# Kernel tuning notes

Hardware: AMD Instinct MI355X
Metric: run time of the kernel (lower is better)

## Reference

```python
import jax, jax.numpy as jnp
import numpy as np

B, T, V, E, U = 64, 256, 32000, 512, 1024


def setup_inputs() -> dict:
    key = jax.random.key(0)
    k1, k2, k3 = jax.random.split(key, 3)
    tokens = jax.random.randint(k1, (B, T), 0, V)
    hidden = jnp.zeros((B, U), dtype=jnp.float32)
    emb = jax.random.normal(k2, (V, E), dtype=jnp.float32) * 0.05
    kx, kh = jax.random.split(k3)
    # Keras GRU v2: kernel [E, 3U], recurrent_kernel [U, 3U], reset_after=True -> two bias vectors
    Wx = jax.random.normal(kx, (E, 3 * U), dtype=jnp.float32) * 0.02
    bx = jnp.zeros((3 * U,), dtype=jnp.float32)
    Wh = jax.random.normal(kh, (U, 3 * U), dtype=jnp.float32) * 0.02
    bh = jnp.zeros((3 * U,), dtype=jnp.float32)
    return {"tokens": tokens, "hidden": hidden, "emb": emb,
            "Wx": Wx, "bx": bx, "Wh": Wh, "bh": bh}


def _gru_scan(x_proj, h0, Wh, bh, units):
    # x_proj: [T, B, 3U] precomputed input projections (incl. input bias)
    def step(h, xt):
        rec = h @ Wh + bh                      # [B, 3U]
        xz, xr, xh = jnp.split(xt, 3, axis=-1)
        hz, hr, hh = jnp.split(rec, 3, axis=-1)
        z = jax.nn.sigmoid(xz + hz)
        r = jax.nn.sigmoid(xr + hr)
        cand = jnp.tanh(xh + r * hh)           # reset_after=True: r applied after matmul
        h_new = z * h + (1.0 - z) * cand
        return h_new, h_new
    h_last, seq = jax.lax.scan(step, h0, x_proj)
    return seq, h_last


def reference(tokens, hidden, emb, Wx, bx, Wh, bh):
    x = emb[tokens]                            # [B, T, E] embedding lookup
    x_proj = jnp.einsum('bte,eu->btu', x, Wx) + bx  # [B, T, 3U]
    seq, h_last = _gru_scan(jnp.swapaxes(x_proj, 0, 1), hidden, Wh, bh, U)
    output = jnp.swapaxes(seq, 0, 1)           # [B, T, U]
    return output, h_last
```

## Files before the change

### kernel.cpp

```cpp
#include <hip/hip_runtime.h>
#include <cstdint>

typedef _Float16 f16x8 __attribute__((ext_vector_type(8)));
typedef float    f32x4 __attribute__((ext_vector_type(4)));
typedef unsigned int u32;

#define BB 64
#define TT 256
#define EE 512
#define UU 1024
#define NN 3072

#define MFMA16(a, b, c) __builtin_amdgcn_mfma_f32_16x16x32_f16((a), (b), (c), 0, 0, 0)

__global__ __launch_bounds__(256) void prep_whf(const float* __restrict__ Wh,
                                                _Float16* __restrict__ WhF) {
    int tid  = blockIdx.x * 256 + threadIdx.x;
    int col8 = tid % 384;
    int k    = tid / 384;
    int kb = k >> 5, quad = (k >> 3) & 3, jj = k & 7;
    const float* src = Wh + (long)k * NN + col8 * 8;
#pragma unroll
    for (int i = 0; i < 8; i++) {
        int n   = col8 * 8 + i;
        int g   = n >> 10;
        int nl  = n & 1023;
        int j   = nl >> 4, l16 = nl & 15;
        int lane = quad * 16 + l16;
        WhF[((((j * 3 + g) * 32 + kb) * 64 + lane) << 3) + jj] = (_Float16)src[i];
    }
}

__global__ __launch_bounds__(256) void prep_h0(const float* __restrict__ h0,
                                               _Float16* __restrict__ hbuf) {
    int i = blockIdx.x * 256 + threadIdx.x;
    hbuf[i] = (_Float16)h0[i];
}

__global__ __launch_bounds__(256) void proj_kernel(
    const int* __restrict__ tokens, const float* __restrict__ emb,
    const float* __restrict__ Wx, const float* __restrict__ bx,
    _Float16* __restrict__ xproj) {
    int tid  = threadIdx.x;
    int wave = tid >> 6, lane = tid & 63, quad = lane >> 4, l16 = lane & 15;
    int bm = blockIdx.x * 64;
    int bn = blockIdx.y * 128;
    int wm = (wave & 1) * 32, wn = (wave >> 1) * 64;

    int row0 = bm + wm + l16;
    const float* a0p = emb + (long)tokens[row0] * EE;
    const float* a1p = emb + (long)tokens[row0 + 16] * EE;

    f32x4 acc[2][4];
#pragma unroll
    for (int mt = 0; mt < 2; mt++)
#pragma unroll
        for (int nt = 0; nt < 4; nt++) { f32x4 z = {0.f, 0.f, 0.f, 0.f}; acc[mt][nt] = z; }

#pragma unroll 2
    for (int k0 = 0; k0 < EE; k0 += 32) {
        int ka = k0 + quad * 8;
        f16x8 afr[2];
        {
            const float4* p = (const float4*)(a0p + ka);
            float4 x0 = p[0], x1 = p[1];
            afr[0][0] = (_Float16)x0.x; afr[0][1] = (_Float16)x0.y;
            afr[0][2] = (_Float16)x0.z; afr[0][3] = (_Float16)x0.w;
            afr[0][4] = (_Float16)x1.x; afr[0][5] = (_Float16)x1.y;
            afr[0][6] = (_Float16)x1.z; afr[0][7] = (_Float16)x1.w;
        }
        {
            const float4* p = (const float4*)(a1p + ka);
            float4 x0 = p[0], x1 = p[1];
            afr[1][0] = (_Float16)x0.x; afr[1][1] = (_Float16)x0.y;
            afr[1][2] = (_Float16)x0.z; afr[1][3] = (_Float16)x0.w;
            afr[1][4] = (_Float16)x1.x; afr[1][5] = (_Float16)x1.y;
            afr[1][6] = (_Float16)x1.z; afr[1][7] = (_Float16)x1.w;
        }
        f16x8 bfr[4];
#pragma unroll
        for (int nt = 0; nt < 4; nt++) {
            const float* bp = Wx + (long)ka * NN + (bn + wn + nt * 16 + l16);
#pragma unroll
            for (int jj = 0; jj < 8; jj++) bfr[nt][jj] = (_Float16)bp[(long)jj * NN];
        }
#pragma unroll
        for (int mt = 0; mt < 2; mt++)
#pragma unroll
            for (int nt = 0; nt < 4; nt++)
                acc[mt][nt] = MFMA16(afr[mt], bfr[nt], acc[mt][nt]);
    }
#pragma unroll
    for (int mt = 0; mt < 2; mt++) {
        int rowbase = bm + wm + mt * 16 + quad * 4;
#pragma unroll
        for (int nt = 0; nt < 4; nt++) {
            int col = bn + wn + nt * 16 + l16;
            float bias = bx[col];
#pragma unroll
            for (int r = 0; r < 4; r++) {
                int i = rowbase + r;
                int b = i >> 8, t = i & 255;
                xproj[((long)t * BB + b) * NN + col] = (_Float16)(acc[mt][nt][r] + bias);
            }
        }
    }
}

__global__ __launch_bounds__(256, 1) void gru_kernel(
    const _Float16* __restrict__ xproj,
    const _Float16* __restrict__ WhF,
    const float* __restrict__ hidden,
    const float* __restrict__ bh,
    _Float16* __restrict__ hbuf,
    u32* cnt,
    float* __restrict__ out) {
    int tid  = threadIdx.x;
    int wave = tid >> 6, lane = tid & 63, quad = lane >> 4, l16 = lane & 15;
    int j  = blockIdx.x;
    int u  = j * 16 + l16;
    int b0 = wave * 16;

    float bhz = bh[u], bhr = bh[UU + u], bhh = bh[2 * UU + u];

    float hold[4];
#pragma unroll
    for (int r = 0; r < 4; r++) hold[r] = hidden[(long)(b0 + quad * 4 + r) * UU + u];

    const f16x8* WF = (const f16x8*)WhF + (long)j * 3 * 32 * 64 + lane;
    f16x8 w[96];
#pragma unroll
    for (int i = 0; i < 96; i++) w[i] = WF[(long)i * 64];
#pragma unroll
    for (int i = 0; i < 64; i++) asm volatile("" : "+a"(w[i]));
#pragma unroll
    for (int i = 64; i < 96; i++) asm volatile("" : "+v"(w[i]));

#pragma unroll 1
    for (int t = 0; t < TT; t++) {
        const _Float16* xp = xproj + (long)t * BB * NN;
        float xzv[4], xrv[4], xhv[4];
#pragma unroll
        for (int r = 0; r < 4; r++) {
            const _Float16* p = xp + (long)(b0 + quad * 4 + r) * NN + u;
            xzv[r] = (float)p[0]; xrv[r] = (float)p[UU]; xhv[r] = (float)p[2 * UU];
        }

        const _Float16* h = hbuf + (long)(t & 1) * BB * UU
                                 + (long)(b0 + l16) * UU + quad * 8;
        f16x8 hf[16];
#pragma unroll
        for (int kb = 0; kb < 16; kb++)
            asm volatile("global_load_dwordx4 %0, %1, off sc0 sc1"
                         : "=v"(hf[kb]) : "v"(h + (long)kb * 32));

        f32x4 az = {0.f, 0.f, 0.f, 0.f}, ar = az, ah = az;
#pragma unroll
        for (int q = 0; q < 4; q++) {
            if (q < 3) asm volatile("s_waitcnt vmcnt(8)" ::: "memory");
            else       asm volatile("s_waitcnt vmcnt(0)" ::: "memory");
            __builtin_amdgcn_sched_barrier(0);
#pragma unroll
            for (int i = 0; i < 8; i++) {
                int kb = q * 8 + i;
                f16x8 afr = hf[kb & 15];
                az = MFMA16(afr, w[kb],      az);
                ar = MFMA16(afr, w[32 + kb], ar);
                ah = MFMA16(afr, w[64 + kb], ah);
            }
            if (q < 2) {
#pragma unroll
                for (int i = 0; i < 8; i++) {
                    int kb2 = 16 + q * 8 + i;
                    asm volatile("global_load_dwordx4 %0, %1, off sc0 sc1"
                                 : "=v"(hf[kb2 & 15]) : "v"(h + (long)kb2 * 32));
                }
            }
        }

        _Float16* hw = hbuf + (long)((t + 1) & 1) * BB * UU;
#pragma unroll
        for (int r = 0; r < 4; r++) {
            int b = b0 + quad * 4 + r;
            float z  = 1.f / (1.f + expf(-(xzv[r] + az[r] + bhz)));
            float rr = 1.f / (1.f + expf(-(xrv[r] + ar[r] + bhr)));
            float cd = tanhf(xhv[r] + rr * (ah[r] + bhh));
            float hn = z * hold[r] + (1.f - z) * cd;
            hold[r] = hn;
            out[(long)b * TT * UU + (long)t * UU + u] = hn;
            u32 hv = (u32)__builtin_bit_cast(unsigned short, (_Float16)hn);
            asm volatile("global_store_short %0, %1, off sc0 sc1"
                         :: "v"(hw + (long)b * UU + u), "v"(hv) : "memory");
        }

        if (t != TT - 1) {
            __syncthreads();
            if (tid == 0) {
                __hip_atomic_fetch_add(cnt + (j >> 3) * 16, 1u,
                                       __ATOMIC_RELAXED, __HIP_MEMORY_SCOPE_AGENT);
                u32 tgt = 8u * (u32)(t + 1);
                for (;;) {
                    u32 c0, c1, c2, c3, c4, c5, c6, c7;
                    asm volatile(
                        "global_load_dword %0, %8, off sc0 sc1\n\t"
                        "global_load_dword %1, %8, off offset:64 sc0 sc1\n\t"
                        "global_load_dword %2, %8, off offset:128 sc0 sc1\n\t"
                        "global_load_dword %3, %8, off offset:192 sc0 sc1\n\t"
                        "global_load_dword %4, %8, off offset:256 sc0 sc1\n\t"
                        "global_load_dword %5, %8, off offset:320 sc0 sc1\n\t"
                        "global_load_dword %6, %8, off offset:384 sc0 sc1\n\t"
                        "global_load_dword %7, %8, off offset:448 sc0 sc1\n\t"
                        "s_waitcnt vmcnt(0)"
                        : "=&v"(c0), "=&v"(c1), "=&v"(c2), "=&v"(c3),
                          "=&v"(c4), "=&v"(c5), "=&v"(c6), "=&v"(c7)
                        : "v"(cnt) : "memory");
                    if (c0 >= tgt && c1 >= tgt && c2 >= tgt && c3 >= tgt &&
                        c4 >= tgt && c5 >= tgt && c6 >= tgt && c7 >= tgt) break;
                    __builtin_amdgcn_s_sleep(1);
                }
            }
            __syncthreads();
        }
    }
#pragma unroll
    for (int r = 0; r < 4; r++) {
        int b = b0 + quad * 4 + r;
        out[(long)BB * TT * UU + (long)b * UU + u] = hold[r];
    }
}

extern "C" void kernel_launch(void* const* d_in, const int* in_sizes, int n_in,
                              void* d_out, int out_size, void* d_ws, size_t ws_size,
                              hipStream_t stream) {
    const int*   tokens = (const int*)d_in[0];
    const float* hidden = (const float*)d_in[1];
    const float* emb    = (const float*)d_in[2];
    const float* Wx     = (const float*)d_in[3];
    const float* bx     = (const float*)d_in[4];
    const float* Wh     = (const float*)d_in[5];
    const float* bh     = (const float*)d_in[6];
    float* out = (float*)d_out;

    char* ws = (char*)d_ws;
    _Float16* xproj = (_Float16*)(ws);
    _Float16* WhF   = (_Float16*)(ws + 100663296L);
    _Float16* hbuf  = (_Float16*)(ws + 106954752L);
    u32*      cnt   = (u32*)(ws + 107216896L);
    if (ws_size < 107217408UL) return;

    hipMemsetAsync(cnt, 0, 512, stream);
    prep_whf<<<1536, 256, 0, stream>>>(Wh, WhF);
    prep_h0<<<256, 256, 0, stream>>>(hidden, hbuf);
    proj_kernel<<<dim3(256, 24), 256, 0, stream>>>(tokens, emb, Wx, bx, xproj);
    gru_kernel<<<64, 256, 0, stream>>>(xproj, WhF, hidden, bh, hbuf, cnt, out);
}
```

Baseline: 2.487 ms.

## Replace atomic step counters with per-block flags and remap block-to-unit order

The inter-block barrier after each timestep no longer does an atomic add on a shared group counter. Each block now stores its own step number into a dedicated flag slot, and 16 lanes poll all 64 flags with vector loads, combined through a wave-wide all-reduce. Block indices are also permuted so that each group of 8 unit-slices maps to blocks with the same `blockIdx & 7`, which likely places a group on one XCD. The aim is lower latency per step from removing atomic contention and serialized polling, at the cost of relying on zero-initialized flags and on cross-block store visibility via sc0 sc1.

```diff
diff --git a/kernel.cpp b/kernel.cpp
--- a/kernel.cpp
+++ b/kernel.cpp
@@ -4,6 +4,7 @@
 typedef _Float16 f16x8 __attribute__((ext_vector_type(8)));
 typedef float    f32x4 __attribute__((ext_vector_type(4)));
 typedef unsigned int u32;
+typedef u32      u32x4 __attribute__((ext_vector_type(4)));
 
 #define BB 64
 #define TT 256
@@ -117,7 +118,7 @@
     float* __restrict__ out) {
     int tid  = threadIdx.x;
     int wave = tid >> 6, lane = tid & 63, quad = lane >> 4, l16 = lane & 15;
-    int j  = blockIdx.x;
+    int j  = ((blockIdx.x & 7) << 3) | (blockIdx.x >> 3);
     int u  = j * 16 + l16;
     int b0 = wave * 16;
 
@@ -135,6 +136,9 @@
     for (int i = 0; i < 64; i++) asm volatile("" : "+a"(w[i]));
 #pragma unroll
     for (int i = 64; i < 96; i++) asm volatile("" : "+v"(w[i]));
+
+    u32* fstore = cnt + ((j >> 3) << 4) + (j & 7);
+    const u32* fpoll = cnt + ((lane >> 1) << 4) + ((lane & 1) << 2);
 
 #pragma unroll 1
     for (int t = 0; t < TT; t++) {
@@ -195,27 +199,19 @@
 
         if (t != TT - 1) {
             __syncthreads();
-            if (tid == 0) {
-                __hip_atomic_fetch_add(cnt + (j >> 3) * 16, 1u,
-                                       __ATOMIC_RELAXED, __HIP_MEMORY_SCOPE_AGENT);
-                u32 tgt = 8u * (u32)(t + 1);
+            if (wave == 0 && lane < 16) {
+                if (lane == 0)
+                    asm volatile("global_store_dword %0, %1, off sc0 sc1"
+                                 :: "v"(fstore), "v"((u32)(t + 1)) : "memory");
+                u32 tgt = (u32)(t + 1);
                 for (;;) {
-                    u32 c0, c1, c2, c3, c4, c5, c6, c7;
-                    asm volatile(
-                        "global_load_dword %0, %8, off sc0 sc1\n\t"
-                        "global_load_dword %1, %8, off offset:64 sc0 sc1\n\t"
-                        "global_load_dword %2, %8, off offset:128 sc0 sc1\n\t"
-                        "global_load_dword %3, %8, off offset:192 sc0 sc1\n\t"
-                        "global_load_dword %4, %8, off offset:256 sc0 sc1\n\t"
-                        "global_load_dword %5, %8, off offset:320 sc0 sc1\n\t"
-                        "global_load_dword %6, %8, off offset:384 sc0 sc1\n\t"
-                        "global_load_dword %7, %8, off offset:448 sc0 sc1\n\t"
-                        "s_waitcnt vmcnt(0)"
-                        : "=&v"(c0), "=&v"(c1), "=&v"(c2), "=&v"(c3),
-                          "=&v"(c4), "=&v"(c5), "=&v"(c6), "=&v"(c7)
-                        : "v"(cnt) : "memory");
-                    if (c0 >= tgt && c1 >= tgt && c2 >= tgt && c3 >= tgt &&
-                        c4 >= tgt && c5 >= tgt && c6 >= tgt && c7 >= tgt) break;
+                    u32x4 fv;
+                    asm volatile("global_load_dwordx4 %0, %1, off sc0 sc1\n\t"
+                                 "s_waitcnt vmcnt(0)"
+                                 : "=v"(fv) : "v"(fpoll) : "memory");
+                    bool ok = (fv[0] >= tgt) & (fv[1] >= tgt) &
+                              (fv[2] >= tgt) & (fv[3] >= tgt);
+                    if (__all(ok)) break;
                     __builtin_amdgcn_s_sleep(1);
                 }
             }
```

New measurement: 2.219 ms. 1.12x faster.
